# Kernel optimization log

Measured on AMD Instinct MI355X. Metric: run time of the kernel, lower is better.

## Reference

```python
import jax, jax.numpy as jnp
import numpy as np

MIN_VAL = float(-2**32 + 1)  # sentinel used to exclude padded cells from top-k
KS = (1, 3, -1)              # default ks; -1 means masked mean pooling


def setup_inputs() -> dict:
    key = jax.random.key(0)
    k1, k2, k3 = jax.random.split(key, 3)
    B, X, Y, C = 32, 128, 256, 64
    inp_mm = jax.random.normal(k1, (B, X, Y, C), dtype=jnp.float32)
    # prefix (padding) masks: ones up to a random valid length
    x_lens = jax.random.randint(k2, (B,), 1, X + 1)
    y_lens = jax.random.randint(k3, (B,), 4, Y + 1)  # >= 4 so top-3 is meaningful
    x_mask = (jnp.arange(X)[None, :] < x_lens[:, None]).astype(jnp.float32)
    y_mask = (jnp.arange(Y)[None, :] < y_lens[:, None]).astype(jnp.float32)
    return {"inp_mm": inp_mm, "x_mask": x_mask, "y_mask": y_mask}


def reference(inp_mm, x_mask, y_mask):
    # inp_mm: [B, X, Y, C]; x_mask: [B, X]; y_mask: [B, Y]
    # joint validity mask, broadcast over channels: [B, X, Y, 1]
    mask = (x_mask[:, :, None] * y_mask[:, None, :])[..., None]
    mm_min = jnp.where(mask == 0, MIN_VAL, inp_mm)   # masked with -inf-like sentinel
    mm_zero = jnp.where(mask == 0, 0.0, inp_mm)      # masked with zeros

    y_real_len = jnp.sum(y_mask, axis=1)[:, None, None]          # [B, 1, 1]
    mean_pool = jnp.sum(mm_zero, axis=2) / y_real_len            # [B, X, C]
    x_mask_exp = x_mask[:, :, None]                              # [B, X, 1]

    topk_in = jnp.transpose(mm_min, (0, 1, 3, 2))                # [B, X, C, Y]
    outs = []
    for k in KS:
        if k == -1:
            outs.append(mean_pool)  # NB: original does not re-mask mean pooling
        else:
            top_k_vals, _ = jax.lax.top_k(topk_in, k)            # [B, X, C, k]
            top_k_mean = jnp.mean(top_k_vals, axis=-1)           # [B, X, C]
            top_k_mean = jnp.where(y_real_len < k, mean_pool, top_k_mean)
            outs.append(top_k_mean * x_mask_exp)
    return jnp.stack(outs, axis=2)  # [B, X, len(KS), C]
```

## Files before the change

### kernel.cpp

```cpp
#include <hip/hip_runtime.h>

#define B_ 32
#define X_ 128
#define Y_ 256
#define C_ 64
#define BDIM 256
#define MIN_VALF -4294967295.0f

__device__ __forceinline__ void insert3(float& m1, float& m2, float& m3, float v) {
    float hi1 = fmaxf(m1, v);
    float lo1 = fminf(m1, v);
    m1 = hi1;
    float hi2 = fmaxf(m2, lo1);
    float lo2 = fminf(m2, lo1);
    m2 = hi2;
    m3 = fmaxf(m3, lo2);
}

__global__ __launch_bounds__(BDIM) void topk_pool_kernel(
    const float* __restrict__ inp,
    const float* __restrict__ xmask,
    const float* __restrict__ ymask,
    float* __restrict__ out)
{
    const int tid  = threadIdx.x;
    const int lane = tid & 63;
    const int wv   = tid >> 6;

    const int w = (blockIdx.x * 1997) & (B_ * X_ - 1);
    const int b = w >> 7;
    const int x = w & (X_ - 1);

    __shared__ float lds[4 * 16 * 16];

    const float xm = xmask[b * X_ + x];
    float* orow = out + (size_t)w * (3 * C_);

    if (xm == 0.0f) {
        if (wv == 0) {
            orow[lane]       = 0.0f;
            orow[64 + lane]  = 0.0f;
            orow[128 + lane] = 0.0f;
        }
        return;
    }

    const float* ym = ymask + b * Y_;
    float ysum = ym[lane] + ym[lane + 64] + ym[lane + 128] + ym[lane + 192];
    #pragma unroll
    for (int off = 32; off > 0; off >>= 1) ysum += __shfl_xor(ysum, off);
    const int   ylen    = (int)(ysum + 0.5f);
    const float inv_len = 1.0f / ysum;

    const int c0   = (lane & 15) << 2;
    const int yofs = lane >> 4;

    float m1[4], m2[4], m3[4], s[4];
    #pragma unroll
    for (int j = 0; j < 4; ++j) {
        m1[j] = MIN_VALF; m2[j] = MIN_VALF; m3[j] = MIN_VALF; s[j] = 0.0f;
    }

    const float* base = inp + (size_t)(b * X_ + x) * (Y_ * C_) + c0;
    const int y_lo = wv * 64;
    const int y0   = y_lo + yofs;

    if (y_lo < ylen) {
        if (y_lo + 64 <= ylen) {
            float4 v[16];
            #pragma unroll
            for (int i = 0; i < 16; ++i)
                v[i] = *reinterpret_cast<const float4*>(base + (size_t)(y0 + 4 * i) * C_);
            #pragma unroll
            for (int i = 0; i < 16; ++i) {
                float vv[4] = {v[i].x, v[i].y, v[i].z, v[i].w};
                #pragma unroll
                for (int j = 0; j < 4; ++j) {
                    s[j] += vv[j];
                    insert3(m1[j], m2[j], m3[j], vv[j]);
                }
            }
        } else {
            float4 v[16];
            #pragma unroll
            for (int i = 0; i < 16; ++i) {
                const int yr = y0 + 4 * i;
                const int yc = (yr < ylen) ? yr : (ylen - 1);
                v[i] = *reinterpret_cast<const float4*>(base + (size_t)yc * C_);
            }
            #pragma unroll
            for (int i = 0; i < 16; ++i) {
                const bool live = (y0 + 4 * i) < ylen;
                float vv[4] = {v[i].x, v[i].y, v[i].z, v[i].w};
                #pragma unroll
                for (int j = 0; j < 4; ++j) {
                    const float vs = live ? vv[j] : 0.0f;
                    const float vt = live ? vv[j] : MIN_VALF;
                    s[j] += vs;
                    insert3(m1[j], m2[j], m3[j], vt);
                }
            }
        }
    }

    #pragma unroll
    for (int step = 0; step < 2; ++step) {
        const int msk = 16 << step;
        #pragma unroll
        for (int j = 0; j < 4; ++j) {
            float o1 = __shfl_xor(m1[j], msk);
            float o2 = __shfl_xor(m2[j], msk);
            float o3 = __shfl_xor(m3[j], msk);
            float os = __shfl_xor(s[j],  msk);
            s[j] += os;
            insert3(m1[j], m2[j], m3[j], o1);
            insert3(m1[j], m2[j], m3[j], o2);
            insert3(m1[j], m2[j], m3[j], o3);
        }
    }

    if (yofs == 0) {
        float* dst = &lds[(wv * 16 + (lane & 15)) * 16];
        *reinterpret_cast<float4*>(dst +  0) = make_float4(m1[0], m1[1], m1[2], m1[3]);
        *reinterpret_cast<float4*>(dst +  4) = make_float4(m2[0], m2[1], m2[2], m2[3]);
        *reinterpret_cast<float4*>(dst +  8) = make_float4(m3[0], m3[1], m3[2], m3[3]);
        *reinterpret_cast<float4*>(dst + 12) = make_float4(s[0],  s[1],  s[2],  s[3]);
    }
    __syncthreads();

    if (wv == 0) {
        const int ch = lane, lg = ch >> 2, e = ch & 3;
        float M1 = MIN_VALF, M2 = MIN_VALF, M3 = MIN_VALF, S = 0.0f;
        #pragma unroll
        for (int q = 0; q < 4; ++q) {
            const float* src = &lds[(q * 16 + lg) * 16];
            float a = src[e], bb = src[4 + e], c = src[8 + e], d = src[12 + e];
            S += d;
            insert3(M1, M2, M3, a);
            insert3(M1, M2, M3, bb);
            insert3(M1, M2, M3, c);
        }
        const float mean = S * inv_len;
        const float top1 = ((ylen >= 1) ? M1 : mean) * xm;
        const float top3 = ((ylen >= 3) ? (M1 + M2 + M3) * (1.0f / 3.0f) : mean) * xm;
        orow[ch]       = top1;
        orow[64 + ch]  = top3;
        orow[128 + ch] = mean;
    }
}

extern "C" void kernel_launch(void* const* d_in, const int* in_sizes, int n_in,
                              void* d_out, int out_size, void* d_ws, size_t ws_size,
                              hipStream_t stream) {
    const float* inp   = (const float*)d_in[0];
    const float* xmask = (const float*)d_in[1];
    const float* ymask = (const float*)d_in[2];
    float* out = (float*)d_out;

    const int grid = B_ * X_;
    topk_pool_kernel<<<grid, BDIM, 0, stream>>>(inp, xmask, ymask, out);
}
```

Measured before the change: 20.83 us.

## Process eight rows per block with double-buffered register prefetch

Changes the kernel from one (b,x) row per block to eight rows per persistent block, with two register buffers so loads for the next row are issued while the current row is reduced. The y-mask lengths for all batches are computed once per block into shared memory, replacing the per-row reduction. This reduces block launch overhead and hides memory latency. In exchange it doubles register pressure, which may lower occupancy, and it launches only 512 blocks.

```diff
diff --git a/kernel.cpp b/kernel.cpp
--- a/kernel.cpp
+++ b/kernel.cpp
@@ -5,6 +5,8 @@
 #define Y_ 256
 #define C_ 64
 #define BDIM 256
+#define NITEM 8
+#define NBLK  (B_ * X_ / NITEM)
 #define MIN_VALF -4294967295.0f
 
 __device__ __forceinline__ void insert3(float& m1, float& m2, float& m3, float v) {
@@ -17,6 +19,118 @@
     m3 = fmaxf(m3, lo2);
 }
 
+struct St {
+    int   w;
+    int   ylen;
+    float inv_len;
+    float xm;
+    bool  alive;
+    bool  loads;
+};
+
+__device__ __forceinline__ void issue_item(
+    int g, int wv, int yofs, int c0,
+    const float* __restrict__ inp, const float* __restrict__ xmask,
+    const float* __restrict__ ylen_lds,
+    St& st, float4 (&buf)[16])
+{
+    const int w = (g * 1997) & (B_ * X_ - 1);
+    const int b = w >> 7;
+    const int x = w & (X_ - 1);
+    st.w  = w;
+    st.xm = xmask[b * X_ + x];
+    const float yf = ylen_lds[b];
+    st.ylen    = (int)(yf + 0.5f);
+    st.inv_len = 1.0f / yf;
+    st.alive   = (st.xm != 0.0f);
+    st.loads   = st.alive && (wv * 64 < st.ylen);
+    if (st.loads) {
+        const float* base = inp + ((size_t)w << 14) + c0;
+        const int y0     = wv * 64 + yofs;
+        const int yc_max = st.ylen - 1;
+        #pragma unroll
+        for (int i = 0; i < 16; ++i) {
+            const int yr = y0 + 4 * i;
+            const int yc = (yr < st.ylen) ? yr : yc_max;
+            buf[i] = *reinterpret_cast<const float4*>(base + ((size_t)yc << 6));
+        }
+    }
+}
+
+__device__ __forceinline__ void consume_item(
+    const St& st, int wv, int yofs, int lane,
+    float4 (&buf)[16], float* ldsp)
+{
+    float m1[4], m2[4], m3[4], s[4];
+    #pragma unroll
+    for (int j = 0; j < 4; ++j) {
+        m1[j] = MIN_VALF; m2[j] = MIN_VALF; m3[j] = MIN_VALF; s[j] = 0.0f;
+    }
+
+    if (st.loads) {
+        const int y0 = wv * 64 + yofs;
+        #pragma unroll
+        for (int i = 0; i < 16; ++i) {
+            const bool live = (y0 + 4 * i) < st.ylen;
+            float vv[4] = {buf[i].x, buf[i].y, buf[i].z, buf[i].w};
+            #pragma unroll
+            for (int j = 0; j < 4; ++j) {
+                s[j] += live ? vv[j] : 0.0f;
+                insert3(m1[j], m2[j], m3[j], live ? vv[j] : MIN_VALF);
+            }
+        }
+    }
+    if (st.alive) {
+        #pragma unroll
+        for (int step = 0; step < 2; ++step) {
+            const int msk = 16 << step;
+            #pragma unroll
+            for (int j = 0; j < 4; ++j) {
+                float o1 = __shfl_xor(m1[j], msk);
+                float o2 = __shfl_xor(m2[j], msk);
+                float o3 = __shfl_xor(m3[j], msk);
+                float os = __shfl_xor(s[j],  msk);
+                s[j] += os;
+                insert3(m1[j], m2[j], m3[j], o1);
+                insert3(m1[j], m2[j], m3[j], o2);
+                insert3(m1[j], m2[j], m3[j], o3);
+            }
+        }
+        if (yofs == 0) {
+            float* dst = ldsp + (wv * 16 + (lane & 15)) * 16;
+            *reinterpret_cast<float4*>(dst +  0) = make_float4(m1[0], m1[1], m1[2], m1[3]);
+            *reinterpret_cast<float4*>(dst +  4) = make_float4(m2[0], m2[1], m2[2], m2[3]);
+            *reinterpret_cast<float4*>(dst +  8) = make_float4(m3[0], m3[1], m3[2], m3[3]);
+            *reinterpret_cast<float4*>(dst + 12) = make_float4(s[0],  s[1],  s[2],  s[3]);
+        }
+    }
+}
+
+__device__ __forceinline__ void finalize_item(
+    const St st, int lane, const float* ldsp, float* __restrict__ out)
+{
+    float* orow = out + (size_t)st.w * (3 * C_);
+    if (!st.alive) {
+        orow[lane] = 0.0f; orow[64 + lane] = 0.0f; orow[128 + lane] = 0.0f;
+        return;
+    }
+    const int lg = lane >> 2, e = lane & 3;
+    float M1 = MIN_VALF, M2 = MIN_VALF, M3 = MIN_VALF, S = 0.0f;
+    #pragma unroll
+    for (int q = 0; q < 4; ++q) {
+        const float* src = ldsp + (q * 16 + lg) * 16;
+        float a = src[e], bb = src[4 + e], c = src[8 + e], d = src[12 + e];
+        S += d;
+        insert3(M1, M2, M3, a);
+        insert3(M1, M2, M3, bb);
+        insert3(M1, M2, M3, c);
+    }
+    const float mean = S * st.inv_len;
+    orow[lane]       = M1 * st.xm;
+    orow[64 + lane]  = ((st.ylen >= 3) ? (M1 + M2 + M3) * (1.0f / 3.0f) : mean) * st.xm;
+    orow[128 + lane] = mean;
+}
+
 __global__ __launch_bounds__(BDIM) void topk_pool_kernel(
     const float* __restrict__ inp,
     const float* __restrict__ xmask,
@@ -26,126 +140,51 @@
     const int tid  = threadIdx.x;
     const int lane = tid & 63;
     const int wv   = tid >> 6;
-
-    const int w = (blockIdx.x * 1997) & (B_ * X_ - 1);
-    const int b = w >> 7;
-    const int x = w & (X_ - 1);
-
-    __shared__ float lds[4 * 16 * 16];
-
-    const float xm = xmask[b * X_ + x];
-    float* orow = out + (size_t)w * (3 * C_);
-
-    if (xm == 0.0f) {
-        if (wv == 0) {
-            orow[lane]       = 0.0f;
-            orow[64 + lane]  = 0.0f;
-            orow[128 + lane] = 0.0f;
-        }
-        return;
-    }
-
-    const float* ym = ymask + b * Y_;
-    float ysum = ym[lane] + ym[lane + 64] + ym[lane + 128] + ym[lane + 192];
-    #pragma unroll
-    for (int off = 32; off > 0; off >>= 1) ysum += __shfl_xor(ysum, off);
-    const int   ylen    = (int)(ysum + 0.5f);
-    const float inv_len = 1.0f / ysum;
-
     const int c0   = (lane & 15) << 2;
     const int yofs = lane >> 4;
 
-    float m1[4], m2[4], m3[4], s[4];
-    #pragma unroll
-    for (int j = 0; j < 4; ++j) {
-        m1[j] = MIN_VALF; m2[j] = MIN_VALF; m3[j] = MIN_VALF; s[j] = 0.0f;
-    }
-
-    const float* base = inp + (size_t)(b * X_ + x) * (Y_ * C_) + c0;
-    const int y_lo = wv * 64;
-    const int y0   = y_lo + yofs;
-
-    if (y_lo < ylen) {
-        if (y_lo + 64 <= ylen) {
-            float4 v[16];
-            #pragma unroll
-            for (int i = 0; i < 16; ++i)
-                v[i] = *reinterpret_cast<const float4*>(base + (size_t)(y0 + 4 * i) * C_);
-            #pragma unroll
-            for (int i = 0; i < 16; ++i) {
-                float vv[4] = {v[i].x, v[i].y, v[i].z, v[i].w};
-                #pragma unroll
-                for (int j = 0; j < 4; ++j) {
-                    s[j] += vv[j];
-                    insert3(m1[j], m2[j], m3[j], vv[j]);
-                }
-            }
-        } else {
-            float4 v[16];
-            #pragma unroll
-            for (int i = 0; i < 16; ++i) {
-                const int yr = y0 + 4 * i;
-                const int yc = (yr < ylen) ? yr : (ylen - 1);
-                v[i] = *reinterpret_cast<const float4*>(base + (size_t)yc * C_);
-            }
-            #pragma unroll
-            for (int i = 0; i < 16; ++i) {
-                const bool live = (y0 + 4 * i) < ylen;
-                float vv[4] = {v[i].x, v[i].y, v[i].z, v[i].w};
-                #pragma unroll
-                for (int j = 0; j < 4; ++j) {
-                    const float vs = live ? vv[j] : 0.0f;
-                    const float vt = live ? vv[j] : MIN_VALF;
-                    s[j] += vs;
-                    insert3(m1[j], m2[j], m3[j], vt);
-                }
-            }
-        }
-    }
-
-    #pragma unroll
-    for (int step = 0; step < 2; ++step) {
-        const int msk = 16 << step;
-        #pragma unroll
-        for (int j = 0; j < 4; ++j) {
-            float o1 = __shfl_xor(m1[j], msk);
-            float o2 = __shfl_xor(m2[j], msk);
-            float o3 = __shfl_xor(m3[j], msk);
-            float os = __shfl_xor(s[j],  msk);
-            s[j] += os;
-            insert3(m1[j], m2[j], m3[j], o1);
-            insert3(m1[j], m2[j], m3[j], o2);
-            insert3(m1[j], m2[j], m3[j], o3);
-        }
-    }
-
-    if (yofs == 0) {
-        float* dst = &lds[(wv * 16 + (lane & 15)) * 16];
-        *reinterpret_cast<float4*>(dst +  0) = make_float4(m1[0], m1[1], m1[2], m1[3]);
-        *reinterpret_cast<float4*>(dst +  4) = make_float4(m2[0], m2[1], m2[2], m2[3]);
-        *reinterpret_cast<float4*>(dst +  8) = make_float4(m3[0], m3[1], m3[2], m3[3]);
-        *reinterpret_cast<float4*>(dst + 12) = make_float4(s[0],  s[1],  s[2],  s[3]);
+    __shared__ float ylen_lds[B_];
+    __shared__ float yps[8][B_];
+    __shared__ float lds0[4 * 16 * 16];
+    __shared__ float lds1[4 * 16 * 16];
+
+    {
+        const int bq = tid & 31, seg = tid >> 5;
+        const float4* yv = reinterpret_cast<const float4*>(ymask + bq * Y_ + seg * 32);
+        float ps = 0.0f;
+        #pragma unroll
+        for (int k = 0; k < 8; ++k) { float4 q = yv[k]; ps += q.x + q.y + q.z + q.w; }
+        yps[seg][bq] = ps;
     }
     __syncthreads();
-
-    if (wv == 0) {
-        const int ch = lane, lg = ch >> 2, e = ch & 3;
-        float M1 = MIN_VALF, M2 = MIN_VALF, M3 = MIN_VALF, S = 0.0f;
-        #pragma unroll
-        for (int q = 0; q < 4; ++q) {
-            const float* src = &lds[(q * 16 + lg) * 16];
-            float a = src[e], bb = src[4 + e], c = src[8 + e], d = src[12 + e];
-            S += d;
-            insert3(M1, M2, M3, a);
-            insert3(M1, M2, M3, bb);
-            insert3(M1, M2, M3, c);
-        }
-        const float mean = S * inv_len;
-        const float top1 = ((ylen >= 1) ? M1 : mean) * xm;
-        const float top3 = ((ylen >= 3) ? (M1 + M2 + M3) * (1.0f / 3.0f) : mean) * xm;
-        orow[ch]       = top1;
-        orow[64 + ch]  = top3;
-        orow[128 + ch] = mean;
+    if (tid < B_) {
+        float sacc = 0.0f;
+        #pragma unroll
+        for (int k = 0; k < 8; ++k) sacc += yps[k][tid];
+        ylen_lds[tid] = sacc;
+    }
+    __syncthreads();
+
+    const int g0 = blockIdx.x * NITEM;
+    St stA, stB;
+    float4 bufA[16], bufB[16];
+    issue_item(g0 + 0, wv, yofs, c0, inp, xmask, ylen_lds, stA, bufA);
+    issue_item(g0 + 1, wv, yofs, c0, inp, xmask, ylen_lds, stB, bufB);
+
+    for (int i = 0; i < NITEM; i += 2) {
+        consume_item(stA, wv, yofs, lane, bufA, lds0);
+        St snapA = stA;
+        if (i + 2 < NITEM)
+            issue_item(g0 + i + 2, wv, yofs, c0, inp, xmask, ylen_lds, stA, bufA);
+        __syncthreads();
+        if (wv == 0) finalize_item(snapA, lane, lds0, out);
+
+        consume_item(stB, wv, yofs, lane, bufB, lds1);
+        St snapB = stB;
+        if (i + 3 < NITEM)
+            issue_item(g0 + i + 3, wv, yofs, c0, inp, xmask, ylen_lds, stB, bufB);
+        __syncthreads();
+        if (wv == 0) finalize_item(snapB, lane, lds1, out);
     }
 }
 
@@ -157,6 +196,5 @@
     const float* ymask = (const float*)d_in[2];
     float* out = (float*)d_out;
 
-    const int grid = B_ * X_;
-    topk_pool_kernel<<<grid, BDIM, 0, stream>>>(inp, xmask, ymask, out);
-}
+    topk_pool_kernel<<<NBLK, BDIM, 0, stream>>>(inp, xmask, ymask, out);
+}
```

Measured after the change: 28.29 us. 1.36x slower.

## Process four rows per block with double-buffered register prefetch

Applied to the files above, without the earlier changes.

Each block now handles four (b,x) rows instead of one, cutting the grid to a quarter. Loads for the next row are issued into two register buffers while the current row is reduced, and the cross-wave LDS staging is double-buffered, so memory latency overlaps with compute. The cost is more registers (launch bounds now ask for 4 blocks/CU), fewer blocks to hide latency, and conditional paths that may serialise.

```diff
diff --git a/kernel.cpp b/kernel.cpp
--- a/kernel.cpp
+++ b/kernel.cpp
@@ -5,6 +5,8 @@
 #define Y_ 256
 #define C_ 64
 #define BDIM 256
+#define NIT 4
+#define NBLK (B_ * X_ / NIT)
 #define MIN_VALF -4294967295.0f
 
 __device__ __forceinline__ void insert3(float& m1, float& m2, float& m3, float v) {
@@ -17,7 +19,33 @@
     m3 = fmaxf(m3, lo2);
 }
 
-__global__ __launch_bounds__(BDIM) void topk_pool_kernel(
+__device__ __forceinline__ void issue8(const float* __restrict__ base, int y0, int ylen,
+                                       float4 (&buf)[8], int k0) {
+    const int ymax = ylen - 1;
+    #pragma unroll
+    for (int k = 0; k < 8; ++k) {
+        const int yr = y0 + 4 * (k0 + k);
+        const int yc = (yr < ylen) ? yr : ymax;
+        buf[k] = *reinterpret_cast<const float4*>(base + ((size_t)yc << 6));
+    }
+}
+
+__device__ __forceinline__ void consume8(int y0, int ylen, const float4 (&buf)[8], int k0,
+                                         float (&m1)[4], float (&m2)[4], float (&m3)[4],
+                                         float (&s)[4]) {
+    #pragma unroll
+    for (int k = 0; k < 8; ++k) {
+        const bool live = (y0 + 4 * (k0 + k)) < ylen;
+        float vv[4] = {buf[k].x, buf[k].y, buf[k].z, buf[k].w};
+        #pragma unroll
+        for (int j = 0; j < 4; ++j) {
+            s[j] += live ? vv[j] : 0.0f;
+            insert3(m1[j], m2[j], m3[j], live ? vv[j] : MIN_VALF);
+        }
+    }
+}
+
+__global__ __launch_bounds__(BDIM, 4) void topk_pool_kernel(
     const float* __restrict__ inp,
     const float* __restrict__ xmask,
     const float* __restrict__ ymask,
@@ -26,126 +54,119 @@
     const int tid  = threadIdx.x;
     const int lane = tid & 63;
     const int wv   = tid >> 6;
-
-    const int w = (blockIdx.x * 1997) & (B_ * X_ - 1);
-    const int b = w >> 7;
-    const int x = w & (X_ - 1);
-
-    __shared__ float lds[4 * 16 * 16];
-
-    const float xm = xmask[b * X_ + x];
-    float* orow = out + (size_t)w * (3 * C_);
-
-    if (xm == 0.0f) {
-        if (wv == 0) {
-            orow[lane]       = 0.0f;
-            orow[64 + lane]  = 0.0f;
-            orow[128 + lane] = 0.0f;
-        }
-        return;
-    }
-
-    const float* ym = ymask + b * Y_;
-    float ysum = ym[lane] + ym[lane + 64] + ym[lane + 128] + ym[lane + 192];
-    #pragma unroll
-    for (int off = 32; off > 0; off >>= 1) ysum += __shfl_xor(ysum, off);
-    const int   ylen    = (int)(ysum + 0.5f);
-    const float inv_len = 1.0f / ysum;
-
     const int c0   = (lane & 15) << 2;
     const int yofs = lane >> 4;
 
-    float m1[4], m2[4], m3[4], s[4];
-    #pragma unroll
-    for (int j = 0; j < 4; ++j) {
-        m1[j] = MIN_VALF; m2[j] = MIN_VALF; m3[j] = MIN_VALF; s[j] = 0.0f;
+    __shared__ float lds[2][4 * 16 * 16];
+
+    int   wA [NIT + 1];
+    float xmA[NIT + 1];
+    int   ylA[NIT + 1];
+    float invA[NIT + 1];
+    {
+        float ys[NIT];
+        #pragma unroll
+        for (int i = 0; i < NIT; ++i) {
+            const int g = blockIdx.x * NIT + i;
+            const int w = (g * 1997) & (B_ * X_ - 1);
+            wA[i] = w;
+            const int b = w >> 7, x = w & (X_ - 1);
+            xmA[i] = xmask[b * X_ + x];
+            const float* ym = ymask + b * Y_;
+            ys[i] = ym[lane] + ym[lane + 64] + ym[lane + 128] + ym[lane + 192];
+        }
+        #pragma unroll
+        for (int i = 0; i < NIT; ++i) {
+            float t = ys[i];
+            #pragma unroll
+            for (int off = 32; off > 0; off >>= 1) t += __shfl_xor(t, off);
+            ylA[i]  = (int)(t + 0.5f);
+            invA[i] = 1.0f / t;
+        }
+        wA[NIT] = 0; xmA[NIT] = 0.0f; ylA[NIT] = 64; invA[NIT] = 0.0f;
     }
 
-    const float* base = inp + (size_t)(b * X_ + x) * (Y_ * C_) + c0;
-    const int y_lo = wv * 64;
-    const int y0   = y_lo + yofs;
+    const int y0 = wv * 64 + yofs;
+    float4 bufA[8], bufB[8];
 
-    if (y_lo < ylen) {
-        if (y_lo + 64 <= ylen) {
-            float4 v[16];
-            #pragma unroll
-            for (int i = 0; i < 16; ++i)
-                v[i] = *reinterpret_cast<const float4*>(base + (size_t)(y0 + 4 * i) * C_);
-            #pragma unroll
-            for (int i = 0; i < 16; ++i) {
-                float vv[4] = {v[i].x, v[i].y, v[i].z, v[i].w};
-                #pragma unroll
-                for (int j = 0; j < 4; ++j) {
-                    s[j] += vv[j];
-                    insert3(m1[j], m2[j], m3[j], vv[j]);
-                }
-            }
-        } else {
-            float4 v[16];
-            #pragma unroll
-            for (int i = 0; i < 16; ++i) {
-                const int yr = y0 + 4 * i;
-                const int yc = (yr < ylen) ? yr : (ylen - 1);
-                v[i] = *reinterpret_cast<const float4*>(base + (size_t)yc * C_);
-            }
-            #pragma unroll
-            for (int i = 0; i < 16; ++i) {
-                const bool live = (y0 + 4 * i) < ylen;
-                float vv[4] = {v[i].x, v[i].y, v[i].z, v[i].w};
-                #pragma unroll
-                for (int j = 0; j < 4; ++j) {
-                    const float vs = live ? vv[j] : 0.0f;
-                    const float vt = live ? vv[j] : MIN_VALF;
-                    s[j] += vs;
-                    insert3(m1[j], m2[j], m3[j], vt);
-                }
-            }
+    {
+        const bool l0 = (xmA[0] != 0.0f) && (wv * 64 < ylA[0]);
+        const float* base0 = inp + ((size_t)wA[0] << 14) + c0;
+        if (l0) {
+            issue8(base0, y0, ylA[0], bufA, 0);
+            issue8(base0, y0, ylA[0], bufB, 8);
         }
     }
 
     #pragma unroll
-    for (int step = 0; step < 2; ++step) {
-        const int msk = 16 << step;
+    for (int i = 0; i < NIT; ++i) {
+        const bool alive  = (xmA[i] != 0.0f);
+        const bool loads  = alive && (wv * 64 < ylA[i]);
+        const bool loadsN = (i + 1 < NIT) && (xmA[i + 1] != 0.0f)
+                            && (wv * 64 < ylA[i + 1]);
+        const float* baseN = inp + ((size_t)wA[i + 1] << 14) + c0;
+
+        float m1[4], m2[4], m3[4], s[4];
         #pragma unroll
         for (int j = 0; j < 4; ++j) {
-            float o1 = __shfl_xor(m1[j], msk);
-            float o2 = __shfl_xor(m2[j], msk);
-            float o3 = __shfl_xor(m3[j], msk);
-            float os = __shfl_xor(s[j],  msk);
-            s[j] += os;
-            insert3(m1[j], m2[j], m3[j], o1);
-            insert3(m1[j], m2[j], m3[j], o2);
-            insert3(m1[j], m2[j], m3[j], o3);
+            m1[j] = MIN_VALF; m2[j] = MIN_VALF; m3[j] = MIN_VALF; s[j] = 0.0f;
         }
-    }
 
-    if (yofs == 0) {
-        float* dst = &lds[(wv * 16 + (lane & 15)) * 16];
-        *reinterpret_cast<float4*>(dst +  0) = make_float4(m1[0], m1[1], m1[2], m1[3]);
-        *reinterpret_cast<float4*>(dst +  4) = make_float4(m2[0], m2[1], m2[2], m2[3]);
-        *reinterpret_cast<float4*>(dst +  8) = make_float4(m3[0], m3[1], m3[2], m3[3]);
-        *reinterpret_cast<float4*>(dst + 12) = make_float4(s[0],  s[1],  s[2],  s[3]);
-    }
-    __syncthreads();
+        if (loads)  consume8(y0, ylA[i], bufA, 0, m1, m2, m3, s);
+        if (loadsN) issue8(baseN, y0, ylA[i + 1], bufA, 0);
+        if (loads)  consume8(y0, ylA[i], bufB, 8, m1, m2, m3, s);
+        if (loadsN) issue8(baseN, y0, ylA[i + 1], bufB, 8);
 
-    if (wv == 0) {
-        const int ch = lane, lg = ch >> 2, e = ch & 3;
-        float M1 = MIN_VALF, M2 = MIN_VALF, M3 = MIN_VALF, S = 0.0f;
-        #pragma unroll
-        for (int q = 0; q < 4; ++q) {
-            const float* src = &lds[(q * 16 + lg) * 16];
-            float a = src[e], bb = src[4 + e], c = src[8 + e], d = src[12 + e];
-            S += d;
-            insert3(M1, M2, M3, a);
-            insert3(M1, M2, M3, bb);
-            insert3(M1, M2, M3, c);
+        if (alive) {
+            #pragma unroll
+            for (int step = 0; step < 2; ++step) {
+                const int msk = 16 << step;
+                #pragma unroll
+                for (int j = 0; j < 4; ++j) {
+                    float o1 = __shfl_xor(m1[j], msk);
+                    float o2 = __shfl_xor(m2[j], msk);
+                    float o3 = __shfl_xor(m3[j], msk);
+                    float os = __shfl_xor(s[j],  msk);
+                    s[j] += os;
+                    insert3(m1[j], m2[j], m3[j], o1);
+                    insert3(m1[j], m2[j], m3[j], o2);
+                    insert3(m1[j], m2[j], m3[j], o3);
+                }
+            }
+            if (yofs == 0) {
+                float* dst = &lds[i & 1][(wv * 16 + (lane & 15)) * 16];
+                *reinterpret_cast<float4*>(dst +  0) = make_float4(m1[0], m1[1], m1[2], m1[3]);
+                *reinterpret_cast<float4*>(dst +  4) = make_float4(m2[0], m2[1], m2[2], m2[3]);
+                *reinterpret_cast<float4*>(dst +  8) = make_float4(m3[0], m3[1], m3[2], m3[3]);
+                *reinterpret_cast<float4*>(dst + 12) = make_float4(s[0],  s[1],  s[2],  s[3]);
+            }
         }
-        const float mean = S * inv_len;
-        const float top1 = ((ylen >= 1) ? M1 : mean) * xm;
-        const float top3 = ((ylen >= 3) ? (M1 + M2 + M3) * (1.0f / 3.0f) : mean) * xm;
-        orow[ch]       = top1;
-        orow[64 + ch]  = top3;
-        orow[128 + ch] = mean;
+        __syncthreads();
+
+        if (wv == 0) {
+            float* orow = out + (size_t)wA[i] * (3 * C_);
+            if (!alive) {
+                orow[lane]       = 0.0f;
+                orow[64 + lane]  = 0.0f;
+                orow[128 + lane] = 0.0f;
+            } else {
+                const int lg = lane >> 2, e = lane & 3;
+                float M1 = MIN_VALF, M2 = MIN_VALF, M3 = MIN_VALF, S = 0.0f;
+                #pragma unroll
+                for (int q = 0; q < 4; ++q) {
+                    const float* src = &lds[i & 1][(q * 16 + lg) * 16];
+                    float a = src[e], bb = src[4 + e], c = src[8 + e], d = src[12 + e];
+                    S += d;
+                    insert3(M1, M2, M3, a);
+                    insert3(M1, M2, M3, bb);
+                    insert3(M1, M2, M3, c);
+                }
+                const float mean = S * invA[i];
+                orow[lane]       = M1 * xmA[i];
+                orow[64 + lane]  = ((ylA[i] >= 3) ? (M1 + M2 + M3) * (1.0f / 3.0f) : mean) * xmA[i];
+                orow[128 + lane] = mean;
+            }
+        }
     }
 }
 
@@ -157,6 +178,5 @@
     const float* ymask = (const float*)d_in[2];
     float* out = (float*)d_out;
 
-    const int grid = B_ * X_;
-    topk_pool_kernel<<<grid, BDIM, 0, stream>>>(inp, xmask, ymask, out);
+    topk_pool_kernel<<<NBLK, BDIM, 0, stream>>>(inp, xmask, ymask, out);
 }
```

After: 27.78 us. +33.4%, slower.
